# Kernel optimization log

Measured on AMD Instinct MI355X. Metric: run time of the kernel, lower is better.

Reference implementation:

```python
import jax, jax.numpy as jnp
import numpy as np

NUM_BINS = 15
N = 33_554_432  # number of samples


def setup_inputs() -> dict:
    key = jax.random.key(0)
    k1, k2 = jax.random.split(key)
    probs = jax.random.uniform(k1, (N,), dtype=jnp.float32)
    labels = jax.random.randint(k2, (N,), 0, 2, dtype=jnp.int32)
    return {"probs": probs, "labels": labels}


def reference(probs, labels):
    # bins = linspace(0,1,NUM_BINS+1); element falls in bin b iff
    # probs > b/NUM_BINS and probs <= (b+1)/NUM_BINS  =>  b = ceil(p*NUM_BINS)-1.
    n = probs.shape[0]
    idx = jnp.clip(jnp.ceil(probs * NUM_BINS).astype(jnp.int32) - 1, 0, NUM_BINS - 1)
    # elements with probs <= 0 or > 1 fall in no bin (strict lower on bin 0)
    valid = (probs > 0.0) & (probs <= 1.0)
    w = valid.astype(probs.dtype)
    counts = jax.ops.segment_sum(w, idx, num_segments=NUM_BINS)
    sum_conf = jax.ops.segment_sum(probs * w, idx, num_segments=NUM_BINS)
    sum_acc = jax.ops.segment_sum(labels.astype(probs.dtype) * w, idx, num_segments=NUM_BINS)
    denom = jnp.maximum(counts, 1.0)  # safe divide; empty bins contribute 0
    avg_conf = sum_conf / denom
    avg_acc = sum_acc / denom
    ece = jnp.sum((counts / n) * jnp.abs(avg_acc - avg_conf))
    return ece
```

## Files before the change

kernel.cpp:

```cpp
#include <hip/hip_runtime.h>

#define NUM_BINS 15
#define NB 1024
#define NT 256
#define NCOMP 45

#define INV15 0.066666667f

__device__ __forceinline__ unsigned pack_elem(float pv, int lv, int* bin_out) {
    int bin = (int)ceilf(pv * 15.0f) - 1;
    bin = (min(max(bin, -1), 15)) & 15;
    *bin_out = bin;
    float res = fmaf((float)bin, -INV15, pv);
    float x   = fmaf(res, 4096.0f, 0.5f);
    unsigned rq = (unsigned)fmaxf(x, 0.0f);
    return ((unsigned)lv << 24) + 0x10000u + rq;
}

__device__ __forceinline__ void process4(float4 p, int4 l,
                                         unsigned* hAt, unsigned* hBt, unsigned* reg) {
    int b0, b1, b2, b3;
    unsigned k0 = pack_elem(p.x, l.x, &b0);
    unsigned k1 = pack_elem(p.y, l.y, &b1);
    unsigned k2 = pack_elem(p.z, l.z, &b2);
    unsigned k3 = pack_elem(p.w, l.w, &b3);
    unsigned* ca = hAt + (b0 << 8);
    unsigned* cb = hBt + (b1 << 8);
    unsigned va = *ca;
    unsigned vb = *cb;
    *ca = va + k0;
    *cb = vb + k1;
#pragma unroll
    for (int b = 0; b < 16; ++b) {
        reg[b] += (b2 == b) ? k2 : 0u;
        reg[b] += (b3 == b) ? k3 : 0u;
    }
}

__global__ __launch_bounds__(NT) void ece_partial(
    const float* __restrict__ probs, const int* __restrict__ labels,
    float* __restrict__ ws, int n4)
{
    __shared__ unsigned hA[16 * NT];
    __shared__ unsigned hB[16 * NT];
    const int t = threadIdx.x;

    uint4* a4 = (uint4*)hA;
    uint4* b4 = (uint4*)hB;
#pragma unroll
    for (int i = 0; i < 4; ++i) {
        a4[i * NT + t] = uint4{0u, 0u, 0u, 0u};
        b4[i * NT + t] = uint4{0u, 0u, 0u, 0u};
    }
    __syncthreads();

    unsigned reg[16];
#pragma unroll
    for (int b = 0; b < 16; ++b) reg[b] = 0u;

    const float4* __restrict__ p4 = (const float4*)probs;
    const int4*   __restrict__ l4 = (const int4*)labels;
    unsigned* hAt = hA + t;
    unsigned* hBt = hB + t;
    const int tid    = blockIdx.x * NT + t;
    const int stride = NB * NT;
    const int iters  = n4 / stride;

#pragma unroll 2
    for (int k = 0; k < iters; ++k) {
        const int i = tid + k * stride;
        process4(p4[i], l4[i], hAt, hBt, reg);
    }
    {
        const int i = tid + iters * stride;
        if (i < n4) process4(p4[i], l4[i], hAt, hBt, reg);
    }

#pragma unroll
    for (int b = 0; b < 16; ++b)
        hA[(b << 8) + t] += hB[(b << 8) + t] + reg[b];
    __syncthreads();

    const int r = t >> 4, s = t & 15;
    float csum = 0.f, asum = 0.f, rsum = 0.f;
#pragma unroll
    for (int k = 0; k < 16; ++k) {
        unsigned v = hA[(r << 8) + (s << 4) + k];
        asum += (float)(v >> 24);
        csum += (float)((v >> 16) & 0xFFu);
        rsum += (float)(v & 0xFFFFu);
    }
#pragma unroll
    for (int o = 8; o; o >>= 1) {
        csum += __shfl_down(csum, o);
        asum += __shfl_down(asum, o);
        rsum += __shfl_down(rsum, o);
    }
    if (s == 0 && r < NUM_BINS) {
        float conf = fmaf(csum, (float)r * INV15, rsum * 2.44140625e-4f);
        ws[r * NB + blockIdx.x]                  = csum;
        ws[(NUM_BINS + r) * NB + blockIdx.x]     = asum;
        ws[(2 * NUM_BINS + r) * NB + blockIdx.x] = conf;
    }
}

__global__ __launch_bounds__(1024) void ece_final(
    const float* __restrict__ ws, float* __restrict__ out, float n)
{
    __shared__ float sums[NCOMP];
    const int wave = threadIdx.x >> 6;
    const int lane = threadIdx.x & 63;

    for (int c = wave; c < NCOMP; c += 16) {
        const float4* row4 = (const float4*)(ws + c * NB);
        float s = 0.f;
#pragma unroll
        for (int k = 0; k < NB / 256; ++k) {
            float4 v = row4[lane + (k << 6)];
            s += (v.x + v.y) + (v.z + v.w);
        }
#pragma unroll
        for (int o = 32; o; o >>= 1) s += __shfl_down(s, o);
        if (lane == 0) sums[c] = s;
    }
    __syncthreads();

    if (threadIdx.x == 0) {
        float ece = 0.f;
#pragma unroll
        for (int b = 0; b < NUM_BINS; ++b) {
            float cnt = sums[b];
            float acc = sums[NUM_BINS + b];
            float cf  = sums[2 * NUM_BINS + b];
            float denom = fmaxf(cnt, 1.f);
            ece += (cnt / n) * fabsf(acc / denom - cf / denom);
        }
        out[0] = ece;
    }
}

extern "C" void kernel_launch(void* const* d_in, const int* in_sizes, int n_in,
                              void* d_out, int out_size, void* d_ws, size_t ws_size,
                              hipStream_t stream)
{
    const float* probs  = (const float*)d_in[0];
    const int*   labels = (const int*)d_in[1];
    const int n = in_sizes[0];

    ece_partial<<<NB, NT, 0, stream>>>(probs, labels, (float*)d_ws, n / 4);
    ece_final<<<1, 1024, 0, stream>>>((const float*)d_ws, (float*)d_out, (float)n);
}
```

Baseline: 278.4 us.

## Use a single per-thread LDS histogram, prefetch loads, and double the block count

Replaces the split scheme, which used two LDS histograms plus a 16-entry register histogram updated by a select loop, with one per-thread LDS histogram updated four times per float4. This halves shared memory per block, frees the register array and adds an occupancy hint, aiming to fit more waves per CU on this latency-bound pass. It also adds one-iteration software prefetch of probs and labels, folds the residual arithmetic into one FMA chain without the clamp, and doubles the grid to 2048 blocks. The trade-off is more LDS read-modify-write traffic and possible bank conflicts in exchange for fewer ALU selects. The larger grid also doubles the partial-sum rows the final kernel reads.

```diff
diff --git a/kernel.cpp b/kernel.cpp
--- a/kernel.cpp
+++ b/kernel.cpp
@@ -1,7 +1,7 @@
 #include <hip/hip_runtime.h>
 
 #define NUM_BINS 15
-#define NB 1024
+#define NB 2048
 #define NT 256
 #define NCOMP 45
 
@@ -11,81 +11,64 @@
     int bin = (int)ceilf(pv * 15.0f) - 1;
     bin = (min(max(bin, -1), 15)) & 15;
     *bin_out = bin;
-    float res = fmaf((float)bin, -INV15, pv);
-    float x   = fmaf(res, 4096.0f, 0.5f);
-    unsigned rq = (unsigned)fmaxf(x, 0.0f);
+    float x = fmaf(pv, 4096.0f, fmaf((float)bin, -4096.0f * INV15, 0.5f));
+    unsigned rq = (unsigned)x;
     return ((unsigned)lv << 24) + 0x10000u + rq;
 }
 
-__device__ __forceinline__ void process4(float4 p, int4 l,
-                                         unsigned* hAt, unsigned* hBt, unsigned* reg) {
+__device__ __forceinline__ void process4(float4 p, int4 l, unsigned* histT) {
     int b0, b1, b2, b3;
     unsigned k0 = pack_elem(p.x, l.x, &b0);
     unsigned k1 = pack_elem(p.y, l.y, &b1);
     unsigned k2 = pack_elem(p.z, l.z, &b2);
     unsigned k3 = pack_elem(p.w, l.w, &b3);
-    unsigned* ca = hAt + (b0 << 8);
-    unsigned* cb = hBt + (b1 << 8);
-    unsigned va = *ca;
-    unsigned vb = *cb;
-    *ca = va + k0;
-    *cb = vb + k1;
-#pragma unroll
-    for (int b = 0; b < 16; ++b) {
-        reg[b] += (b2 == b) ? k2 : 0u;
-        reg[b] += (b3 == b) ? k3 : 0u;
-    }
+    histT[b0 << 8] += k0;
+    histT[b1 << 8] += k1;
+    histT[b2 << 8] += k2;
+    histT[b3 << 8] += k3;
 }
 
-__global__ __launch_bounds__(NT) void ece_partial(
+__global__ __launch_bounds__(NT, 8) void ece_partial(
     const float* __restrict__ probs, const int* __restrict__ labels,
     float* __restrict__ ws, int n4)
 {
-    __shared__ unsigned hA[16 * NT];
-    __shared__ unsigned hB[16 * NT];
+    __shared__ unsigned hist[16 * NT];
     const int t = threadIdx.x;
 
-    uint4* a4 = (uint4*)hA;
-    uint4* b4 = (uint4*)hB;
+    uint4* h4 = (uint4*)hist;
 #pragma unroll
-    for (int i = 0; i < 4; ++i) {
-        a4[i * NT + t] = uint4{0u, 0u, 0u, 0u};
-        b4[i * NT + t] = uint4{0u, 0u, 0u, 0u};
-    }
+    for (int i = 0; i < 4; ++i) h4[i * NT + t] = uint4{0u, 0u, 0u, 0u};
     __syncthreads();
-
-    unsigned reg[16];
-#pragma unroll
-    for (int b = 0; b < 16; ++b) reg[b] = 0u;
 
     const float4* __restrict__ p4 = (const float4*)probs;
     const int4*   __restrict__ l4 = (const int4*)labels;
-    unsigned* hAt = hA + t;
-    unsigned* hBt = hB + t;
+    unsigned* histT = hist + t;
     const int tid    = blockIdx.x * NT + t;
     const int stride = NB * NT;
     const int iters  = n4 / stride;
 
-#pragma unroll 2
-    for (int k = 0; k < iters; ++k) {
-        const int i = tid + k * stride;
-        process4(p4[i], l4[i], hAt, hBt, reg);
+    float4 p = p4[tid];
+    int4   l = l4[tid];
+#pragma unroll 1
+    for (int k = 0; k < iters - 1; ++k) {
+        const int i = tid + (k + 1) * stride;
+        float4 pn = p4[i];
+        int4   ln = l4[i];
+        process4(p, l, histT);
+        p = pn; l = ln;
     }
+    process4(p, l, histT);
     {
         const int i = tid + iters * stride;
-        if (i < n4) process4(p4[i], l4[i], hAt, hBt, reg);
+        if (i < n4) process4(p4[i], l4[i], histT);
     }
-
-#pragma unroll
-    for (int b = 0; b < 16; ++b)
-        hA[(b << 8) + t] += hB[(b << 8) + t] + reg[b];
     __syncthreads();
 
     const int r = t >> 4, s = t & 15;
     float csum = 0.f, asum = 0.f, rsum = 0.f;
 #pragma unroll
     for (int k = 0; k < 16; ++k) {
-        unsigned v = hA[(r << 8) + (s << 4) + k];
+        unsigned v = hist[(r << 8) + (s << 4) + k];
         asum += (float)(v >> 24);
         csum += (float)((v >> 16) & 0xFFu);
         rsum += (float)(v & 0xFFFFu);
```

After: 281.6 us. About the same (+1.2%).
